# Kernel tuning notes

Hardware: AMD Instinct MI355X
Metric: run time of the kernel (lower is better)

The kernel has to match this reference:

```python
import math
import jax, jax.numpy as jnp
import numpy as np

B, S, D, H = 4, 2048, 1024, 16
DK = D // H
THETA = 10000.0


def _rope(xh, pos):
    # xh: [B, H, S, DK], pos: [S]
    half = jnp.arange(0, DK, 2, dtype=jnp.float32) / DK
    inv_freq = THETA ** (-half)                      # [DK/2]
    ang = pos.astype(jnp.float32)[:, None] * inv_freq  # [S, DK/2]
    cos, sin = jnp.cos(ang).astype(xh.dtype), jnp.sin(ang).astype(xh.dtype)
    x1, x2 = xh[..., 0::2], xh[..., 1::2]
    r1 = x1 * cos - x2 * sin
    r2 = x1 * sin + x2 * cos
    return jnp.stack([r1, r2], axis=-1).reshape(xh.shape)


def setup_inputs() -> dict:
    key = jax.random.key(0)
    kx, kq, kk, kv, ko = jax.random.split(key, 5)
    std = 0.02
    x = jax.random.normal(kx, (B, S, D), jnp.float32)
    wq = jax.random.normal(kq, (D, D), jnp.float32) * std
    wk = jax.random.normal(kk, (D, D), jnp.float32) * std
    wv = jax.random.normal(kv, (D, D), jnp.float32) * std
    wo = jax.random.normal(ko, (D, D), jnp.float32) * std
    token_positions = jnp.arange(S, dtype=jnp.int32)
    return {"x": x, "wq": wq, "wk": wk, "wv": wv, "wo": wo,
            "token_positions": token_positions}


def reference(x, wq, wk, wv, wo, token_positions):
    # bias-free linear projections: y = x @ W^T (torch Linear convention)
    q = x @ wq.T
    k = x @ wk.T
    v = x @ wv.T
    # split heads: [B, S, D] -> [B, H, S, DK]
    to_heads = lambda t: t.reshape(B, S, H, DK).transpose(0, 2, 1, 3)
    qh, kh, vh = to_heads(q), to_heads(k), to_heads(v)
    qh = _rope(qh, token_positions)
    kh = _rope(kh, token_positions)
    scores = jnp.einsum('bhqd,bhkd->bhqk', qh, kh) / math.sqrt(DK)
    causal = jnp.tril(jnp.ones((S, S), dtype=bool))
    scores = jnp.where(causal, scores, -jnp.inf)
    attn = jax.nn.softmax(scores, axis=-1)
    out = jnp.einsum('bhqk,bhkd->bhqd', attn, vh)       # [B, H, S, DK]
    out = out.transpose(0, 2, 1, 3).reshape(B, S, D)    # merge heads
    return out @ wo.T
```

## Files before the change

### kernel.cpp

```cpp
#include <hip/hip_runtime.h>

#define B_ 4
#define S_ 2048
#define D_ 1024
#define H_ 16
#define DK_ 64
#define M_ (B_*S_)
#define K_ D_
#define N_ D_

typedef unsigned short u16;
typedef unsigned int u32;
typedef __bf16 bf16x8 __attribute__((ext_vector_type(8)));
typedef float f32x4 __attribute__((ext_vector_type(4)));
typedef u32 u32x4v __attribute__((ext_vector_type(4)));

#define EXP2F(x) __builtin_amdgcn_exp2f(x)

__device__ __forceinline__ u16 f2bf(float f) {
    u32 u = __builtin_bit_cast(u32, f);
    u += 0x7fff + ((u >> 16) & 1);
    return (u16)(u >> 16);
}
__device__ __forceinline__ float bf2f(u16 h) {
    u32 u = ((u32)h) << 16;
    return __builtin_bit_cast(float, u);
}
__device__ __forceinline__ u32 pack_trunc(float a, float b) {
    return (__builtin_bit_cast(u32, a) >> 16) | (__builtin_bit_cast(u32, b) & 0xffff0000u);
}

#define GLDS16(g, l) __builtin_amdgcn_global_load_lds( \
    (__attribute__((address_space(1))) void*)(g),      \
    (__attribute__((address_space(3))) void*)(l), 16, 0, 0)

__global__ __launch_bounds__(256) void cvt_x(const float* __restrict__ in,
                                             u16* __restrict__ out, int n4) {
    const int i = blockIdx.x * 256 + threadIdx.x;
    if (i >= n4) return;
    const float4 f = *(const float4*)(in + (size_t)i * 4);
    u32 p0 = (u32)f2bf(f.x) | ((u32)f2bf(f.y) << 16);
    u32 p1 = (u32)f2bf(f.z) | ((u32)f2bf(f.w) << 16);
    *(uint2*)(out + (size_t)i * 4) = make_uint2(p0, p1);
}

__global__ __launch_bounds__(256) void cvt_w4(
    const float* __restrict__ w0, const float* __restrict__ w1,
    const float* __restrict__ w2, const float* __restrict__ w3,
    u16* __restrict__ o0, u16* __restrict__ o1,
    u16* __restrict__ o2, u16* __restrict__ o3) {
    const int wi = blockIdx.y;
    const float* in = (wi == 0) ? w0 : (wi == 1) ? w1 : (wi == 2) ? w2 : w3;
    u16* out       = (wi == 0) ? o0 : (wi == 1) ? o1 : (wi == 2) ? o2 : o3;
    const int i = blockIdx.x * 256 + threadIdx.x;
    const float4 f = *(const float4*)(in + (size_t)i * 4);
    u32 p0 = (u32)f2bf(f.x) | ((u32)f2bf(f.y) << 16);
    u32 p1 = (u32)f2bf(f.z) | ((u32)f2bf(f.w) << 16);
    *(uint2*)(out + (size_t)i * 4) = make_uint2(p0, p1);
}

template <int MODE>
__device__ __forceinline__ void gemm_tile(const u16* __restrict__ A,
                                          const u16* __restrict__ Bm,
                                          void* __restrict__ Cv) {
    __shared__ u16 As[2][128 * 32];
    __shared__ u16 Bs[2][128 * 32];
    const int tid  = threadIdx.x;
    const int wave = tid >> 6, lane = tid & 63;
    const int m0 = blockIdx.y * 128, n0 = blockIdx.x * 128;
    const int wm = wave & 1, wn = wave >> 1;
    const int quad = lane >> 4, mcol = lane & 15;

    const int c0 = wave, c1 = wave + 4;
    const int r0 = c0 * 16 + (lane >> 2), r1 = c1 * 16 + (lane >> 2);
    const int kb = (lane & 3) * 8;
    const u16* ga0 = A  + (size_t)(m0 + r0) * K_ + kb;
    const u16* ga1 = A  + (size_t)(m0 + r1) * K_ + kb;
    const u16* gb0 = Bm + (size_t)(n0 + r0) * K_ + kb;
    const u16* gb1 = Bm + (size_t)(n0 + r1) * K_ + kb;
    const int lo0 = c0 * 512, lo1 = c1 * 512;

    f32x4 acc[4][4];
#pragma unroll
    for (int i = 0; i < 4; i++)
#pragma unroll
        for (int j = 0; j < 4; j++) acc[i][j] = f32x4{0.f, 0.f, 0.f, 0.f};

    GLDS16(ga0, &As[0][lo0]); GLDS16(ga1, &As[0][lo1]);
    GLDS16(gb0, &Bs[0][lo0]); GLDS16(gb1, &Bs[0][lo1]);
    ga0 += 32; ga1 += 32; gb0 += 32; gb1 += 32;
    __syncthreads();

    for (int kt = 0; kt < K_; kt += 32) {
        const int cur = (kt >> 5) & 1;
        if (kt + 32 < K_) {
            const int nxt = cur ^ 1;
            GLDS16(ga0, &As[nxt][lo0]); GLDS16(ga1, &As[nxt][lo1]);
            GLDS16(gb0, &Bs[nxt][lo0]); GLDS16(gb1, &Bs[nxt][lo1]);
            ga0 += 32; ga1 += 32; gb0 += 32; gb1 += 32;
        }

        bf16x8 af[4], bfr[4];
#pragma unroll
        for (int i = 0; i < 4; i++) {
            af[i]  = *(const bf16x8*)&As[cur][(wm * 64 + i * 16 + mcol) * 32 + quad * 8];
            bfr[i] = *(const bf16x8*)&Bs[cur][(wn * 64 + i * 16 + mcol) * 32 + quad * 8];
        }
#pragma unroll
        for (int i = 0; i < 4; i++)
#pragma unroll
            for (int j = 0; j < 4; j++)
                acc[i][j] = __builtin_amdgcn_mfma_f32_16x16x32_bf16(
                    af[i], bfr[j], acc[i][j], 0, 0, 0);

        __syncthreads();
    }

#pragma unroll
    for (int i = 0; i < 4; i++) {
        const int row = m0 + wm * 64 + i * 16 + quad * 4;
#pragma unroll
        for (int j = 0; j < 4; j++) {
            const int col = n0 + wn * 64 + j * 16 + mcol;
            if constexpr (MODE == 2) {
                const int hh = col >> 6, dd = col & 63;
                const int bb = row >> 11, ss = row & 2047;
                const u32 lo = (u32)f2bf(acc[i][j][0]) | ((u32)f2bf(acc[i][j][1]) << 16);
                const u32 hi = (u32)f2bf(acc[i][j][2]) | ((u32)f2bf(acc[i][j][3]) << 16);
                *(uint2*)((u16*)Cv + ((size_t)((bb * H_ + hh) * DK_ + dd)) * S_ + ss) =
                    make_uint2(lo, hi);
            } else {
#pragma unroll
                for (int r = 0; r < 4; r++) {
                    if constexpr (MODE == 1)
                        ((float*)Cv)[(size_t)(row + r) * N_ + col] = acc[i][j][r];
                    else
                        ((u16*)Cv)[(size_t)(row + r) * N_ + col] = f2bf(acc[i][j][r]);
                }
            }
        }
    }
}

__global__ __launch_bounds__(256) void gemm_qkv_kernel(
    const u16* __restrict__ x,
    const u16* __restrict__ wq, const u16* __restrict__ wk,
    const u16* __restrict__ wv,
    u16* __restrict__ q, u16* __restrict__ k, u16* __restrict__ vt) {
    if (blockIdx.z == 2) {
        gemm_tile<2>(x, wv, vt);
    } else {
        const u16* Bm = blockIdx.z ? wk : wq;
        u16* C        = blockIdx.z ? k  : q;
        gemm_tile<0>(x, Bm, C);
    }
}

__global__ __launch_bounds__(256) void gemm_out_kernel(
    const u16* __restrict__ o, const u16* __restrict__ wo, float* __restrict__ out) {
    gemm_tile<1>(o, wo, out);
}

__global__ __launch_bounds__(256) void rope_qk(u16* __restrict__ q,
                                               u16* __restrict__ k,
                                               const int* __restrict__ pos) {
    const int idx = blockIdx.x * 256 + threadIdx.x;
    const int seg = idx & 3;
    const int h = (idx >> 2) & (H_ - 1);
    const int s = (idx >> 6) & (S_ - 1);
    const int b = idx >> 17;
    const float p = (float)pos[s];
    const float QSC = 0.18033688011112042f;
    const size_t off = ((size_t)(b * S_ + s)) * D_ + h * DK_ + seg * 16;

    u32 qa[8], ka[8];
    *(uint4*)&qa[0] = *(const uint4*)(q + off);
    *(uint4*)&qa[4] = *(const uint4*)(q + off + 8);
    *(uint4*)&ka[0] = *(const uint4*)(k + off);
    *(uint4*)&ka[4] = *(const uint4*)(k + off + 8);
#pragma unroll
    for (int w = 0; w < 8; w++) {
        const int i = seg * 8 + w;
        const float inv = exp2f((float)i * (-13.287712379549449f / 32.f));
        const float ang = p * inv;
        float sn, cs;
        __sincosf(ang, &sn, &cs);
        {
            const float x1 = bf2f((u16)(qa[w] & 0xffff));
            const float x2 = bf2f((u16)(qa[w] >> 16));
            qa[w] = (u32)f2bf((x1 * cs - x2 * sn) * QSC) |
                    ((u32)f2bf((x1 * sn + x2 * cs) * QSC) << 16);
        }
        {
            const float x1 = bf2f((u16)(ka[w] & 0xffff));
            const float x2 = bf2f((u16)(ka[w] >> 16));
            ka[w] = (u32)f2bf(x1 * cs - x2 * sn) |
                    ((u32)f2bf(x1 * sn + x2 * cs) << 16);
        }
    }
    *(uint4*)(q + off)     = *(uint4*)&qa[0];
    *(uint4*)(q + off + 8) = *(uint4*)&qa[4];
    *(uint4*)(k + off)     = *(uint4*)&ka[0];
    *(uint4*)(k + off + 8) = *(uint4*)&ka[4];
}

__global__ __launch_bounds__(256) void attn_kernel(
    const u16* __restrict__ q, const u16* __restrict__ k,
    const u16* __restrict__ vt, u16* __restrict__ o) {
    __shared__ u16 Ks[64 * 64];
    __shared__ u16 Vs[64 * 64];

    const int tid = threadIdx.x, wave = tid >> 6, lane = tid & 63;
    const int flat = blockIdx.x;
    const int qp = flat >> 6;
    const int h = flat & (H_ - 1);
    const int b = (flat >> 4) & 3;
    const int quad = lane >> 4, mcol = lane & 15;
    const int srd = mcol & 7;

    const int rr2 = tid >> 2, cc2 = tid & 3;
    const int sw = rr2 & 7;
    const int so0 = rr2 * 64 + (((cc2 * 2)     ^ sw) << 3);
    const int so1 = rr2 * 64 + (((cc2 * 2 + 1) ^ sw) << 3);
    const int prr = (rr2 & 35) | ((rr2 & 12) << 1) | ((rr2 & 16) >> 2);
    const int ch2 = cc2 * 16;
    const u16* krow = k + ((size_t)(b * S_ + prr)) * D_ + h * DK_ + ch2;
    const u16* vrow = vt + ((size_t)((b * H_ + h) * DK_ + rr2)) * S_ + ch2;

    for (int pass = 0; pass < 2; pass++) {
        const int qt = pass ? (15 - qp) : qp;
        const int q0 = qt * 128;
        const int wq0 = q0 + wave * 32;
        const int jmax = 2 * qt + 1;

        bf16x8 qf[2][2];
#pragma unroll
        for (int g = 0; g < 2; g++) {
            const u16* qs = q + ((size_t)(b * S_ + wq0 + g * 16 + mcol)) * D_ + h * DK_ + quad * 8;
            qf[g][0] = *(const bf16x8*)qs;
            qf[g][1] = *(const bf16x8*)(qs + 32);
        }

        float m[2] = {-1e30f, -1e30f}, l[2] = {0.f, 0.f};
        f32x4 oacc[2][4];
#pragma unroll
        for (int g = 0; g < 2; g++)
#pragma unroll
            for (int dn = 0; dn < 4; dn++) oacc[g][dn] = f32x4{0.f, 0.f, 0.f, 0.f};

        uint4 kr0 = *(const uint4*)(krow);
        uint4 kr1 = *(const uint4*)(krow + 8);
        uint4 vr0 = *(const uint4*)(vrow);
        uint4 vr1 = *(const uint4*)(vrow + 8);

        for (int j = 0; j <= jmax; j++) {
            __syncthreads();
            *(uint4*)&Ks[so0] = kr0;
            *(uint4*)&Ks[so1] = kr1;
            *(uint4*)&Vs[so0] = vr0;
            *(uint4*)&Vs[so1] = vr1;
            __syncthreads();

            if (j < jmax) {
                kr0 = *(const uint4*)(krow + (size_t)(j + 1) * 64 * D_);
                kr1 = *(const uint4*)(krow + (size_t)(j + 1) * 64 * D_ + 8);
                vr0 = *(const uint4*)(vrow + (j + 1) * 64);
                vr1 = *(const uint4*)(vrow + (j + 1) * 64 + 8);
            }

            if (j * 64 > wq0 + 31) continue;

            f32x4 st[2][4];
            __builtin_amdgcn_s_setprio(1);
#pragma unroll
            for (int n = 0; n < 4; n++) {
                const u16* kl = &Ks[(n * 16 + mcol) * 64];
                bf16x8 kf0 = *(const bf16x8*)&kl[(quad ^ srd) << 3];
                bf16x8 kf1 = *(const bf16x8*)&kl[((quad | 4) ^ srd) << 3];
                f32x4 z0 = f32x4{0.f, 0.f, 0.f, 0.f};
                z0 = __builtin_amdgcn_mfma_f32_16x16x32_bf16(kf0, qf[0][0], z0, 0, 0, 0);
                z0 = __builtin_amdgcn_mfma_f32_16x16x32_bf16(kf1, qf[0][1], z0, 0, 0, 0);
                st[0][n] = z0;
                f32x4 z1 = f32x4{0.f, 0.f, 0.f, 0.f};
                z1 = __builtin_amdgcn_mfma_f32_16x16x32_bf16(kf0, qf[1][0], z1, 0, 0, 0);
                z1 = __builtin_amdgcn_mfma_f32_16x16x32_bf16(kf1, qf[1][1], z1, 0, 0, 0);
                st[1][n] = z1;
            }
            __builtin_amdgcn_s_setprio(0);

            if (j * 64 + 63 > wq0) {
#pragma unroll
                for (int g = 0; g < 2; g++) {
                    const int qg = wq0 + g * 16 + mcol;
#pragma unroll
                    for (int n = 0; n < 4; n++) {
                        const int tb = j * 64 + ((n >> 1) << 5) + ((n & 1) << 2) + quad * 8;
#pragma unroll
                        for (int r = 0; r < 4; r++)
                            if (tb + r > qg) st[g][n][r] = -1e30f;
                    }
                }
            }

#pragma unroll
            for (int g = 0; g < 2; g++) {
                float mx = st[g][0][0];
#pragma unroll
                for (int n = 0; n < 4; n++)
#pragma unroll
                    for (int r = 0; r < 4; r++) mx = fmaxf(mx, st[g][n][r]);
                mx = fmaxf(mx, __shfl_xor(mx, 16));
                mx = fmaxf(mx, __shfl_xor(mx, 32));
                float al = 1.f;
                const bool need = !__all(mx <= m[g] + 8.f);
                if (need) {
                    const float mnew = fmaxf(m[g], mx);
                    al = EXP2F(m[g] - mnew);
                    m[g] = mnew;
                }
                float sum = 0.f;
#pragma unroll
                for (int n = 0; n < 4; n++)
#pragma unroll
                    for (int r = 0; r < 4; r++) {
                        const float p = EXP2F(st[g][n][r] - m[g]);
                        st[g][n][r] = p;
                        sum += p;
                    }
                sum += __shfl_xor(sum, 16);
                sum += __shfl_xor(sum, 32);
                l[g] = l[g] * al + sum;
                if (need) {
                    float alphaT[4];
#pragma unroll
                    for (int r = 0; r < 4; r++) alphaT[r] = __shfl(al, quad * 4 + r);
#pragma unroll
                    for (int dn = 0; dn < 4; dn++)
#pragma unroll
                        for (int r = 0; r < 4; r++) oacc[g][dn][r] *= alphaT[r];
                }
            }

            bf16x8 pf[2][2];
#pragma unroll
            for (int g = 0; g < 2; g++) {
                u32x4v w0, w1;
                w0[0] = pack_trunc(st[g][0][0], st[g][0][1]);
                w0[1] = pack_trunc(st[g][0][2], st[g][0][3]);
                w0[2] = pack_trunc(st[g][1][0], st[g][1][1]);
                w0[3] = pack_trunc(st[g][1][2], st[g][1][3]);
                w1[0] = pack_trunc(st[g][2][0], st[g][2][1]);
                w1[1] = pack_trunc(st[g][2][2], st[g][2][3]);
                w1[2] = pack_trunc(st[g][3][0], st[g][3][1]);
                w1[3] = pack_trunc(st[g][3][2], st[g][3][3]);
                pf[g][0] = __builtin_bit_cast(bf16x8, w0);
                pf[g][1] = __builtin_bit_cast(bf16x8, w1);
            }

            __builtin_amdgcn_s_setprio(1);
#pragma unroll
            for (int dn = 0; dn < 4; dn++) {
                const u16* vl = &Vs[(dn * 16 + mcol) * 64];
                bf16x8 vf0 = *(const bf16x8*)&vl[(quad ^ srd) << 3];
                bf16x8 vf1 = *(const bf16x8*)&vl[((quad | 4) ^ srd) << 3];
#pragma unroll
                for (int g = 0; g < 2; g++) {
                    oacc[g][dn] = __builtin_amdgcn_mfma_f32_16x16x32_bf16(pf[g][0], vf0, oacc[g][dn], 0, 0, 0);
                    oacc[g][dn] = __builtin_amdgcn_mfma_f32_16x16x32_bf16(pf[g][1], vf1, oacc[g][dn], 0, 0, 0);
                }
            }
            __builtin_amdgcn_s_setprio(0);
        }

#pragma unroll
        for (int g = 0; g < 2; g++) {
            float linv[4];
#pragma unroll
            for (int r = 0; r < 4; r++) linv[r] = 1.f / __shfl(l[g], quad * 4 + r);
#pragma unroll
            for (int dn = 0; dn < 4; dn++)
#pragma unroll
                for (int r = 0; r < 4; r++) {
                    const int row = wq0 + g * 16 + quad * 4 + r;
                    o[((size_t)(b * S_ + row)) * D_ + h * DK_ + dn * 16 + mcol] =
                        f2bf(oacc[g][dn][r] * linv[r]);
                }
        }
    }
}

extern "C" void kernel_launch(void* const* d_in, const int* in_sizes, int n_in,
                              void* d_out, int out_size, void* d_ws, size_t ws_size,
                              hipStream_t stream) {
    const float* x  = (const float*)d_in[0];
    const float* wq = (const float*)d_in[1];
    const float* wk = (const float*)d_in[2];
    const float* wv = (const float*)d_in[3];
    const float* wo = (const float*)d_in[4];
    const int*   tp = (const int*)d_in[5];
    float* out = (float*)d_out;

    u16* ws = (u16*)d_ws;
    const size_t NE = (size_t)M_ * D_;
    const size_t WE = (size_t)N_ * K_;
    u16* xb  = ws;
    u16* wqb = ws + NE;
    u16* wkb = wqb + WE;
    u16* wvb = wkb + WE;
    u16* wob = wvb + WE;
    u16* qb  = wob + WE;
    u16* kb  = qb + NE;
    u16* vtb = (u16*)d_out;
    u16* ob  = xb;

    dim3 blk(256);
    cvt_x<<<dim3((int)(NE / 1024)), blk, 0, stream>>>(x, xb, (int)(NE / 4));
    cvt_w4<<<dim3((int)(WE / 1024), 4), blk, 0, stream>>>(wq, wk, wv, wo, wqb, wkb, wvb, wob);

    gemm_qkv_kernel<<<dim3(N_ / 128, M_ / 128, 3), blk, 0, stream>>>(xb, wqb, wkb, wvb, qb, kb, vtb);
    rope_qk<<<dim3((B_ * S_ * H_ * 4) / 256), blk, 0, stream>>>(qb, kb, tp);
    attn_kernel<<<dim3((S_ / 128 / 2) * H_ * B_), blk, 0, stream>>>(qb, kb, vtb, ob);
    gemm_out_kernel<<<dim3(N_ / 128, M_ / 128, 1), blk, 0, stream>>>(ob, wob, out);
}
```

Baseline: 275.6 us.

## Swizzle GEMM LDS tiles and remap blocks for XCD-aware scheduling

Applies an XOR swizzle to the k-chunk position used when staging A/B tiles into LDS, and the matching swizzle when reading MFMA fragments, to cut LDS bank conflicts on the 64-byte-row tiles. It also flattens the GEMM launch grids to 1D and remaps block ids so that blocks dispatched round-robin across the 8 XCDs get contiguous tile ranges, which should improve L2 reuse of the A and B operands. The cost is extra index arithmetic, and correctness depends on the load-side and read-side swizzles matching.

New measurement: 266.9 us. 3.1% less time.

```diff
diff --git a/kernel.cpp b/kernel.cpp
--- a/kernel.cpp
+++ b/kernel.cpp
@@ -62,23 +62,24 @@
 template <int MODE>
 __device__ __forceinline__ void gemm_tile(const u16* __restrict__ A,
                                           const u16* __restrict__ Bm,
-                                          void* __restrict__ Cv) {
+                                          void* __restrict__ Cv,
+                                          int m0, int n0) {
     __shared__ u16 As[2][128 * 32];
     __shared__ u16 Bs[2][128 * 32];
     const int tid  = threadIdx.x;
     const int wave = tid >> 6, lane = tid & 63;
-    const int m0 = blockIdx.y * 128, n0 = blockIdx.x * 128;
     const int wm = wave & 1, wn = wave >> 1;
     const int quad = lane >> 4, mcol = lane & 15;
 
     const int c0 = wave, c1 = wave + 4;
     const int r0 = c0 * 16 + (lane >> 2), r1 = c1 * 16 + (lane >> 2);
-    const int kb = (lane & 3) * 8;
+    const int kb = (((lane & 3) ^ ((lane >> 3) & 3)) * 8);
     const u16* ga0 = A  + (size_t)(m0 + r0) * K_ + kb;
     const u16* ga1 = A  + (size_t)(m0 + r1) * K_ + kb;
     const u16* gb0 = Bm + (size_t)(n0 + r0) * K_ + kb;
     const u16* gb1 = Bm + (size_t)(n0 + r1) * K_ + kb;
     const int lo0 = c0 * 512, lo1 = c1 * 512;
+    const int rsw = ((mcol >> 1) & 3);
 
     f32x4 acc[4][4];
 #pragma unroll
@@ -103,8 +104,8 @@
         bf16x8 af[4], bfr[4];
 #pragma unroll
         for (int i = 0; i < 4; i++) {
-            af[i]  = *(const bf16x8*)&As[cur][(wm * 64 + i * 16 + mcol) * 32 + quad * 8];
-            bfr[i] = *(const bf16x8*)&Bs[cur][(wn * 64 + i * 16 + mcol) * 32 + quad * 8];
+            af[i]  = *(const bf16x8*)&As[cur][(wm * 64 + i * 16 + mcol) * 32 + ((quad ^ rsw)) * 8];
+            bfr[i] = *(const bf16x8*)&Bs[cur][(wn * 64 + i * 16 + mcol) * 32 + ((quad ^ rsw)) * 8];
         }
 #pragma unroll
         for (int i = 0; i < 4; i++)
@@ -147,18 +148,27 @@
     const u16* __restrict__ wq, const u16* __restrict__ wk,
     const u16* __restrict__ wv,
     u16* __restrict__ q, u16* __restrict__ k, u16* __restrict__ vt) {
-    if (blockIdx.z == 2) {
-        gemm_tile<2>(x, wv, vt);
+    const int flat = blockIdx.x;
+    const int w = (flat & 7) * 192 + (flat >> 3);
+    const int my = w / 24;
+    const int rem = w - my * 24;
+    const int z = rem >> 3, nx = rem & 7;
+    const int m0 = my * 128, n0 = nx * 128;
+    if (z == 2) {
+        gemm_tile<2>(x, wv, vt, m0, n0);
     } else {
-        const u16* Bm = blockIdx.z ? wk : wq;
-        u16* C        = blockIdx.z ? k  : q;
-        gemm_tile<0>(x, Bm, C);
+        const u16* Bm = z ? wk : wq;
+        u16* C        = z ? k  : q;
+        gemm_tile<0>(x, Bm, C, m0, n0);
     }
 }
 
 __global__ __launch_bounds__(256) void gemm_out_kernel(
     const u16* __restrict__ o, const u16* __restrict__ wo, float* __restrict__ out) {
-    gemm_tile<1>(o, wo, out);
+    const int flat = blockIdx.x;
+    const int w = (flat & 7) * 64 + (flat >> 3);
+    const int my = w >> 3, nx = w & 7;
+    gemm_tile<1>(o, wo, out, my * 128, nx * 128);
 }
 
 __global__ __launch_bounds__(256) void rope_qk(u16* __restrict__ q,
@@ -417,8 +427,8 @@
     cvt_x<<<dim3((int)(NE / 1024)), blk, 0, stream>>>(x, xb, (int)(NE / 4));
     cvt_w4<<<dim3((int)(WE / 1024), 4), blk, 0, stream>>>(wq, wk, wv, wo, wqb, wkb, wvb, wob);
 
-    gemm_qkv_kernel<<<dim3(N_ / 128, M_ / 128, 3), blk, 0, stream>>>(xb, wqb, wkb, wvb, qb, kb, vtb);
+    gemm_qkv_kernel<<<dim3(3 * (M_ / 128) * (N_ / 128)), blk, 0, stream>>>(xb, wqb, wkb, wvb, qb, kb, vtb);
     rope_qk<<<dim3((B_ * S_ * H_ * 4) / 256), blk, 0, stream>>>(qb, kb, tp);
     attn_kernel<<<dim3((S_ / 128 / 2) * H_ * B_), blk, 0, stream>>>(qb, kb, vtb, ob);
-    gemm_out_kernel<<<dim3(N_ / 128, M_ / 128, 1), blk, 0, stream>>>(ob, wob, out);
-}
+    gemm_out_kernel<<<dim3((M_ / 128) * (N_ / 128)), blk, 0, stream>>>(ob, wob, out);
+}
```
